# Optimization experiments

Hardware: AMD Instinct MI355X
Metric: run time of the kernel (lower is better)

Reference implementation:

```python
import jax, jax.numpy as jnp
import numpy as np

WIN_SIZE = 11
WIN_SIGMA = 1.5
DATA_RANGE = 1.0
K1, K2 = 0.01, 0.03


def _gauss_1d(size, sigma):
    coords = np.arange(size, dtype=np.float64) - size // 2
    g = np.exp(-(coords ** 2) / (2.0 * sigma ** 2))
    g = g / g.sum()
    return jnp.asarray(g, dtype=jnp.float32)


def _gaussian_filter(x, win1d):
    # x: (N, C, H, W); separable depthwise gaussian blur, VALID padding
    C = x.shape[1]
    dn = ('NCHW', 'OIHW', 'NCHW')
    kh = jnp.tile(win1d.reshape(1, 1, -1, 1), (C, 1, 1, 1))
    kw = jnp.tile(win1d.reshape(1, 1, 1, -1), (C, 1, 1, 1))
    x = jax.lax.conv_general_dilated(x, kh, (1, 1), 'VALID', dimension_numbers=dn, feature_group_count=C)
    x = jax.lax.conv_general_dilated(x, kw, (1, 1), 'VALID', dimension_numbers=dn, feature_group_count=C)
    return x


def setup_inputs() -> dict:
    key = jax.random.key(0)
    k1, k2 = jax.random.split(key)
    shape = (32, 1, 512, 512)
    y_pred = jax.random.uniform(k1, shape, dtype=jnp.float32)
    y_true = jax.random.uniform(k2, shape, dtype=jnp.float32)
    return {"y_pred": y_pred, "y_true": y_true}


def reference(y_pred, y_true):
    # SSIMLoss.forward: 1 - ssim(y_true, y_pred, data_range=1.0, size_average=True)
    C1 = (K1 * DATA_RANGE) ** 2
    C2 = (K2 * DATA_RANGE) ** 2
    win = _gauss_1d(WIN_SIZE, WIN_SIGMA)

    X, Y = y_true, y_pred
    mu1 = _gaussian_filter(X, win)
    mu2 = _gaussian_filter(Y, win)
    sigma1_sq = _gaussian_filter(X * X, win) - mu1 * mu1
    sigma2_sq = _gaussian_filter(Y * Y, win) - mu2 * mu2
    sigma12 = _gaussian_filter(X * Y, win) - mu1 * mu2

    cs_map = (2.0 * sigma12 + C2) / (sigma1_sq + sigma2_sq + C2)
    ssim_map = ((2.0 * mu1 * mu2 + C1) / (mu1 * mu1 + mu2 * mu2 + C1)) * cs_map
    # size_average=True -> mean over everything
    return 1.0 - jnp.mean(ssim_map)
```

## Files before the change

kernel.cpp:

```cpp
#include <hip/hip_runtime.h>
#include <cmath>

#define IMG      512
#define OUT      502
#define TW       64
#define TH       32
#define IW       74
#define PITCH    76
#define NTHREADS 256
#define TILES_X  8
#define TILES_Y  16
#define NIMG     32
#define NBLOCKS  (TILES_X * TILES_Y * NIMG)

struct GaussW { float w[11]; };

__global__ __launch_bounds__(NTHREADS, 4)
void ssim_tile_kernel(const float* __restrict__ ypred,
                      const float* __restrict__ ytrue,
                      float* __restrict__ partials,
                      GaussW gw)
{
    __shared__ __align__(16) float sV[5][TH * PITCH];
    __shared__ float wsum[4];

    const int t     = threadIdx.x;
    const int tileX = blockIdx.x, tileY = blockIdx.y, img = blockIdx.z;
    const int ox0   = tileX * TW;
    const int oy0   = tileY * TH;

    const float* __restrict__ Xp = ytrue + (size_t)img * IMG * IMG;
    const float* __restrict__ Yp = ypred + (size_t)img * IMG * IMG;

    if (t < IW * 3) {
        const int c    = t % IW;
        const int g    = t / IW;
        const int r0   = g * 11;
        const int jmax = (g == 2) ? 10 : 11;

        int gx = ox0 + c; if (gx > IMG - 1) gx = IMG - 1;
        const float* __restrict__ Xc = Xp + gx;
        const float* __restrict__ Yc = Yp + gx;

        float acc[5][11];
        #pragma unroll
        for (int m = 0; m < 5; ++m)
            #pragma unroll
            for (int j = 0; j < 11; ++j) acc[m][j] = 0.f;

        #pragma unroll
        for (int k = 0; k < 21; ++k) {
            int gy = oy0 + r0 + k; if (gy > IMG - 1) gy = IMG - 1;
            const float x = Xc[(size_t)gy * IMG];
            const float y = Yc[(size_t)gy * IMG];
            const float xx = x * x, yy = y * y, xy = x * y;
            #pragma unroll
            for (int j = 0; j < 11; ++j) {
                if (k - j >= 0 && k - j <= 10) {
                    const float w = gw.w[k - j];
                    acc[0][j] += w * x;
                    acc[1][j] += w * y;
                    acc[2][j] += w * xx;
                    acc[3][j] += w * yy;
                    acc[4][j] += w * xy;
                }
            }
        }

        #pragma unroll
        for (int j = 0; j < 11; ++j) {
            if (j < jmax) {
                const int o = (r0 + j) * PITCH + c;
                sV[0][o] = acc[0][j];
                sV[1][o] = acc[1][j];
                sV[2][o] = acc[2][j];
                sV[3][o] = acc[3][j];
                sV[4][o] = acc[4][j];
            }
        }
    }
    __syncthreads();

    const float C1 = 0.0001f;
    const float C2 = 0.0009f;
    float lsum = 0.f;

    #pragma unroll
    for (int it = 0; it < 2; ++it) {
        const int i   = t + it * NTHREADS;
        const int cg  = i & 15;
        const int row = i >> 4;

        float res[5][4];
        #pragma unroll
        for (int m = 0; m < 5; ++m) {
            const float4* p = reinterpret_cast<const float4*>(&sV[m][row * PITCH + cg * 4]);
            const float4 a = p[0], b = p[1], cq = p[2], d = p[3];
            const float win[16] = { a.x,  a.y,  a.z,  a.w,
                                    b.x,  b.y,  b.z,  b.w,
                                    cq.x, cq.y, cq.z, cq.w,
                                    d.x,  d.y,  d.z,  d.w };
            #pragma unroll
            for (int c = 0; c < 4; ++c) {
                float r = 0.f;
                #pragma unroll
                for (int k = 0; k < 11; ++k) r += gw.w[k] * win[c + k];
                res[m][c] = r;
            }
        }

        const int oy = oy0 + row;
        #pragma unroll
        for (int c = 0; c < 4; ++c) {
            const int ox = ox0 + cg * 4 + c;
            const float mu1 = res[0][c], mu2 = res[1][c];
            const float s1  = res[2][c] - mu1 * mu1;
            const float s2  = res[3][c] - mu2 * mu2;
            const float s12 = res[4][c] - mu1 * mu2;
            const float num = (2.f * mu1 * mu2 + C1) * (2.f * s12 + C2);
            const float den = (mu1 * mu1 + mu2 * mu2 + C1) * (s1 + s2 + C2);
            const float ssim = num / den;
            if (ox < OUT && oy < OUT) lsum += ssim;
        }
    }

    #pragma unroll
    for (int off = 32; off > 0; off >>= 1) lsum += __shfl_down(lsum, off, 64);
    if ((t & 63) == 0) wsum[t >> 6] = lsum;
    __syncthreads();
    if (t == 0) {
        const float b = wsum[0] + wsum[1] + wsum[2] + wsum[3];
        partials[((size_t)img * TILES_Y + tileY) * TILES_X + tileX] = b;
    }
}

__global__ void ssim_reduce_kernel(const float* __restrict__ partials,
                                   float* __restrict__ out)
{
    __shared__ double ws[4];
    const int t = threadIdx.x;
    double s = 0.0;
    for (int i = t; i < NBLOCKS; i += 256) s += (double)partials[i];
    #pragma unroll
    for (int off = 32; off > 0; off >>= 1) s += __shfl_down(s, off, 64);
    if ((t & 63) == 0) ws[t >> 6] = s;
    __syncthreads();
    if (t == 0) {
        const double total = ws[0] + ws[1] + ws[2] + ws[3];
        const double mean  = total / ((double)OUT * (double)OUT * (double)NIMG);
        out[0] = (float)(1.0 - mean);
    }
}

extern "C" void kernel_launch(void* const* d_in, const int* in_sizes, int n_in,
                              void* d_out, int out_size, void* d_ws, size_t ws_size,
                              hipStream_t stream)
{
    const float* ypred = (const float*)d_in[0];
    const float* ytrue = (const float*)d_in[1];
    float* out      = (float*)d_out;
    float* partials = (float*)d_ws;

    GaussW gw;
    double g[11], sum = 0.0;
    for (int i = 0; i < 11; ++i) {
        const double c = (double)i - 5.0;
        g[i] = std::exp(-(c * c) / (2.0 * 1.5 * 1.5));
        sum += g[i];
    }
    for (int i = 0; i < 11; ++i) gw.w[i] = (float)(g[i] / sum);

    dim3 grid(TILES_X, TILES_Y, NIMG);
    ssim_tile_kernel<<<grid, NTHREADS, 0, stream>>>(ypred, ytrue, partials, gw);
    ssim_reduce_kernel<<<1, 256, 0, stream>>>(partials, out);
}
```

Measured before the change: 130.1 us.

## Shift edge tiles inward and widen horizontal pass to 8 outputs per thread

Measured after the change: 127.4 us. 2.1% less time.

```diff
diff --git a/kernel.cpp b/kernel.cpp
--- a/kernel.cpp
+++ b/kernel.cpp
@@ -7,6 +7,7 @@
 #define TH       32
 #define IW       74
 #define PITCH    76
+#define MOFF     (TH * PITCH)
 #define NTHREADS 256
 #define TILES_X  8
 #define TILES_Y  16
@@ -15,32 +16,31 @@
 
 struct GaussW { float w[11]; };
 
-__global__ __launch_bounds__(NTHREADS, 4)
+__global__ __launch_bounds__(NTHREADS, 3)
 void ssim_tile_kernel(const float* __restrict__ ypred,
                       const float* __restrict__ ytrue,
                       float* __restrict__ partials,
                       GaussW gw)
 {
-    __shared__ __align__(16) float sV[5][TH * PITCH];
+    __shared__ __align__(16) float sV[5 * MOFF];
     __shared__ float wsum[4];
 
     const int t     = threadIdx.x;
     const int tileX = blockIdx.x, tileY = blockIdx.y, img = blockIdx.z;
-    const int ox0   = tileX * TW;
-    const int oy0   = tileY * TH;
+    const int ox0 = (tileX == TILES_X - 1) ? (OUT - TW) : tileX * TW;
+    const int oy0 = (tileY == TILES_Y - 1) ? (OUT - TH) : tileY * TH;
 
-    const float* __restrict__ Xp = ytrue + (size_t)img * IMG * IMG;
-    const float* __restrict__ Yp = ypred + (size_t)img * IMG * IMG;
+    const size_t imgoff = (size_t)img * (IMG * IMG);
+    const float* __restrict__ Xp = ytrue + imgoff;
+    const float* __restrict__ Yp = ypred + imgoff;
 
     if (t < IW * 3) {
-        const int c    = t % IW;
-        const int g    = t / IW;
-        const int r0   = g * 11;
-        const int jmax = (g == 2) ? 10 : 11;
+        const int c  = t % IW;
+        const int g  = t / IW;
+        const int r0 = g * 11;
 
-        int gx = ox0 + c; if (gx > IMG - 1) gx = IMG - 1;
-        const float* __restrict__ Xc = Xp + gx;
-        const float* __restrict__ Yc = Yp + gx;
+        const float* __restrict__ Xc = Xp + (size_t)(oy0 + r0) * IMG + (ox0 + c);
+        const float* __restrict__ Yc = Yp + (size_t)(oy0 + r0) * IMG + (ox0 + c);
 
         float acc[5][11];
         #pragma unroll
@@ -49,10 +49,9 @@
             for (int j = 0; j < 11; ++j) acc[m][j] = 0.f;
 
         #pragma unroll
-        for (int k = 0; k < 21; ++k) {
-            int gy = oy0 + r0 + k; if (gy > IMG - 1) gy = IMG - 1;
-            const float x = Xc[(size_t)gy * IMG];
-            const float y = Yc[(size_t)gy * IMG];
+        for (int k = 0; k < 20; ++k) {
+            const float x = Xc[k * IMG];
+            const float y = Yc[k * IMG];
             const float xx = x * x, yy = y * y, xy = x * y;
             #pragma unroll
             for (int j = 0; j < 11; ++j) {
@@ -66,62 +65,83 @@
                 }
             }
         }
+        if (g < 2) {
+            const float x = Xc[20 * IMG];
+            const float y = Yc[20 * IMG];
+            const float w = gw.w[10];
+            acc[0][10] += w * x;
+            acc[1][10] += w * y;
+            acc[2][10] += w * (x * x);
+            acc[3][10] += w * (y * y);
+            acc[4][10] += w * (x * y);
+        }
 
+        const int o0 = r0 * PITCH + c;
         #pragma unroll
-        for (int j = 0; j < 11; ++j) {
-            if (j < jmax) {
-                const int o = (r0 + j) * PITCH + c;
-                sV[0][o] = acc[0][j];
-                sV[1][o] = acc[1][j];
-                sV[2][o] = acc[2][j];
-                sV[3][o] = acc[3][j];
-                sV[4][o] = acc[4][j];
-            }
+        for (int j = 0; j < 10; ++j) {
+            const int o = o0 + j * PITCH;
+            sV[0 * MOFF + o] = acc[0][j];
+            sV[1 * MOFF + o] = acc[1][j];
+            sV[2 * MOFF + o] = acc[2][j];
+            sV[3 * MOFF + o] = acc[3][j];
+            sV[4 * MOFF + o] = acc[4][j];
+        }
+        if (g < 2) {
+            const int o = o0 + 10 * PITCH;
+            sV[0 * MOFF + o] = acc[0][10];
+            sV[1 * MOFF + o] = acc[1][10];
+            sV[2 * MOFF + o] = acc[2][10];
+            sV[3 * MOFF + o] = acc[3][10];
+            sV[4 * MOFF + o] = acc[4][10];
         }
     }
     __syncthreads();
 
     const float C1 = 0.0001f;
     const float C2 = 0.0009f;
+
+    const int row  = t & 31;
+    const int seg  = t >> 5;
+    const int base = row * PITCH + seg * 8;
+
+    float res[5][8];
+    #pragma unroll
+    for (int m = 0; m < 5; ++m) {
+        const float4 q0 = *reinterpret_cast<const float4*>(&sV[base + m * MOFF +  0]);
+        const float4 q1 = *reinterpret_cast<const float4*>(&sV[base + m * MOFF +  4]);
+        const float4 q2 = *reinterpret_cast<const float4*>(&sV[base + m * MOFF +  8]);
+        const float4 q3 = *reinterpret_cast<const float4*>(&sV[base + m * MOFF + 12]);
+        const float4 q4 = *reinterpret_cast<const float4*>(&sV[base + m * MOFF + 16]);
+        const float win[20] = { q0.x, q0.y, q0.z, q0.w,
+                                q1.x, q1.y, q1.z, q1.w,
+                                q2.x, q2.y, q2.z, q2.w,
+                                q3.x, q3.y, q3.z, q3.w,
+                                q4.x, q4.y, q4.z, q4.w };
+        #pragma unroll
+        for (int c = 0; c < 8; ++c) {
+            float r = 0.f;
+            #pragma unroll
+            for (int k = 0; k < 11; ++k) r += gw.w[k] * win[c + k];
+            res[m][c] = r;
+        }
+    }
+
+    const int  oy     = oy0 + row;
+    const bool rowown = (oy >= tileY * TH);
     float lsum = 0.f;
 
     #pragma unroll
-    for (int it = 0; it < 2; ++it) {
-        const int i   = t + it * NTHREADS;
-        const int cg  = i & 15;
-        const int row = i >> 4;
-
-        float res[5][4];
-        #pragma unroll
-        for (int m = 0; m < 5; ++m) {
-            const float4* p = reinterpret_cast<const float4*>(&sV[m][row * PITCH + cg * 4]);
-            const float4 a = p[0], b = p[1], cq = p[2], d = p[3];
-            const float win[16] = { a.x,  a.y,  a.z,  a.w,
-                                    b.x,  b.y,  b.z,  b.w,
-                                    cq.x, cq.y, cq.z, cq.w,
-                                    d.x,  d.y,  d.z,  d.w };
-            #pragma unroll
-            for (int c = 0; c < 4; ++c) {
-                float r = 0.f;
-                #pragma unroll
-                for (int k = 0; k < 11; ++k) r += gw.w[k] * win[c + k];
-                res[m][c] = r;
-            }
-        }
-
-        const int oy = oy0 + row;
-        #pragma unroll
-        for (int c = 0; c < 4; ++c) {
-            const int ox = ox0 + cg * 4 + c;
-            const float mu1 = res[0][c], mu2 = res[1][c];
-            const float s1  = res[2][c] - mu1 * mu1;
-            const float s2  = res[3][c] - mu2 * mu2;
-            const float s12 = res[4][c] - mu1 * mu2;
-            const float num = (2.f * mu1 * mu2 + C1) * (2.f * s12 + C2);
-            const float den = (mu1 * mu1 + mu2 * mu2 + C1) * (s1 + s2 + C2);
-            const float ssim = num / den;
-            if (ox < OUT && oy < OUT) lsum += ssim;
-        }
+    for (int c = 0; c < 8; ++c) {
+        const int  ox  = ox0 + seg * 8 + c;
+        const bool own = rowown && (ox >= tileX * TW);
+        const float mu1 = res[0][c], mu2 = res[1][c];
+        const float s1  = res[2][c] - mu1 * mu1;
+        const float s2  = res[3][c] - mu2 * mu2;
+        const float s12 = res[4][c] - mu1 * mu2;
+        const float num = (2.f * mu1 * mu2 + C1) * (2.f * s12 + C2);
+        const float den = (mu1 * mu1 + mu2 * mu2 + C1) * (s1 + s2 + C2);
+        const float ssim = num / den;
+        lsum += own ? ssim : 0.f;
     }
 
     #pragma unroll
```

## Compute separable Gaussian blur with bf16 MFMA using split hi/lo precision

Applied to the files above, without the earlier changes.

Measured after the change: 159.6 us. 22.7% more time.

```diff
diff --git a/kernel.cpp b/kernel.cpp
--- a/kernel.cpp
+++ b/kernel.cpp
@@ -2,135 +2,188 @@
 #include <cmath>
 
 #define IMG      512
-#define OUT      502
+#define OUTD     502
 #define TW       64
-#define TH       32
-#define IW       74
-#define PITCH    76
+#define TH       16
 #define NTHREADS 256
 #define TILES_X  8
-#define TILES_Y  16
+#define TILES_Y  32
 #define NIMG     32
 #define NBLOCKS  (TILES_X * TILES_Y * NIMG)
-
-struct GaussW { float w[11]; };
-
-__global__ __launch_bounds__(NTHREADS, 4)
-void ssim_tile_kernel(const float* __restrict__ ypred,
+#define HT_PITCH 32
+
+typedef float f32x4  __attribute__((ext_vector_type(4)));
+typedef short bf16x8 __attribute__((ext_vector_type(8)));
+
+struct WSplit { unsigned short hi[11]; unsigned short lo[11]; };
+
+union Frag { unsigned u[4]; bf16x8 v; };
+
+__device__ __forceinline__ unsigned fbits(float x) { return __builtin_bit_cast(unsigned, x); }
+__device__ __forceinline__ float truncbf(float x) {
+    return __builtin_bit_cast(float, fbits(x) & 0xFFFF0000u);
+}
+__device__ __forceinline__ unsigned pkhi(float a, float b) {
+    return (fbits(b) & 0xFFFF0000u) | (fbits(a) >> 16);
+}
+__device__ __forceinline__ void split8(const float* v, Frag& fh, Frag& fl) {
+    #pragma unroll
+    for (int j = 0; j < 4; ++j) {
+        const float a = v[2*j], b = v[2*j+1];
+        fh.u[j] = pkhi(a, b);
+        fl.u[j] = pkhi(a - truncbf(a), b - truncbf(b));
+    }
+}
+
+#define MFMA16 __builtin_amdgcn_mfma_f32_16x16x32_bf16
+
+__global__ __launch_bounds__(NTHREADS, 3)
+void ssim_mfma_kernel(const float* __restrict__ ypred,
                       const float* __restrict__ ytrue,
                       float* __restrict__ partials,
-                      GaussW gw)
+                      WSplit ws)
 {
-    __shared__ __align__(16) float sV[5][TH * PITCH];
+    __shared__ unsigned short Wh[16][32], Wl[16][32];
+    __shared__ unsigned short Hp[10][TW * HT_PITCH];
     __shared__ float wsum[4];
 
-    const int t     = threadIdx.x;
-    const int tileX = blockIdx.x, tileY = blockIdx.y, img = blockIdx.z;
-    const int ox0   = tileX * TW;
-    const int oy0   = tileY * TH;
-
-    const float* __restrict__ Xp = ytrue + (size_t)img * IMG * IMG;
-    const float* __restrict__ Yp = ypred + (size_t)img * IMG * IMG;
-
-    if (t < IW * 3) {
-        const int c    = t % IW;
-        const int g    = t / IW;
-        const int r0   = g * 11;
-        const int jmax = (g == 2) ? 10 : 11;
-
-        int gx = ox0 + c; if (gx > IMG - 1) gx = IMG - 1;
-        const float* __restrict__ Xc = Xp + gx;
-        const float* __restrict__ Yc = Yp + gx;
-
-        float acc[5][11];
-        #pragma unroll
-        for (int m = 0; m < 5; ++m)
-            #pragma unroll
-            for (int j = 0; j < 11; ++j) acc[m][j] = 0.f;
-
-        #pragma unroll
-        for (int k = 0; k < 21; ++k) {
-            int gy = oy0 + r0 + k; if (gy > IMG - 1) gy = IMG - 1;
-            const float x = Xc[(size_t)gy * IMG];
-            const float y = Yc[(size_t)gy * IMG];
-            const float xx = x * x, yy = y * y, xy = x * y;
-            #pragma unroll
-            for (int j = 0; j < 11; ++j) {
-                if (k - j >= 0 && k - j <= 10) {
-                    const float w = gw.w[k - j];
-                    acc[0][j] += w * x;
-                    acc[1][j] += w * y;
-                    acc[2][j] += w * xx;
-                    acc[3][j] += w * yy;
-                    acc[4][j] += w * xy;
-                }
-            }
+    const int t    = threadIdx.x;
+    const int w    = t >> 6;
+    const int lane = t & 63;
+    const int m16  = lane & 15;
+    const int g4   = lane >> 4;
+
+    const int ox0 = blockIdx.x * TW;
+    const int oy0 = blockIdx.y * TH;
+    const int img = blockIdx.z;
+
+    const size_t imgoff = (size_t)img * (IMG * IMG);
+    const float* __restrict__ Xp = ytrue + imgoff;
+    const float* __restrict__ Yp = ypred + imgoff;
+
+    #pragma unroll
+    for (int i = t; i < 512; i += NTHREADS) {
+        const int n = i >> 5, k = i & 31, j = k - n;
+        const bool in = (j >= 0) && (j <= 10);
+        Wh[n][k] = in ? ws.hi[j] : 0;
+        Wl[n][k] = in ? ws.lo[j] : 0;
+    }
+    __syncthreads();
+
+    Frag wfh, wfl;
+    wfh.v = *reinterpret_cast<const bf16x8*>(&Wh[m16][g4 * 8]);
+    wfl.v = *reinterpret_cast<const bf16x8*>(&Wl[m16][g4 * 8]);
+
+    #pragma unroll
+    for (int u = 0; u < 2; ++u) {
+        const int uid = w * 2 + u;
+        const int rg  = uid >> 2;
+        const int ncg = uid & 3;
+
+        const int lrow = rg * 16 + m16;
+        const int grow = min(oy0 + lrow, IMG - 1);
+        const float* __restrict__ Xr = Xp + (size_t)grow * IMG;
+        const float* __restrict__ Yr = Yp + (size_t)grow * IMG;
+        const int cb = ox0 + ncg * 16 + g4 * 8;
+
+        float xv[8], yv[8];
+        #pragma unroll
+        for (int j = 0; j < 4; ++j) {
+            const int c = min(cb + 2 * j, IMG - 2);
+            const float2 fx = *reinterpret_cast<const float2*>(Xr + c);
+            const float2 fy = *reinterpret_cast<const float2*>(Yr + c);
+            xv[2*j] = fx.x; xv[2*j+1] = fx.y;
+            yv[2*j] = fy.x; yv[2*j+1] = fy.y;
         }
 
-        #pragma unroll
-        for (int j = 0; j < 11; ++j) {
-            if (j < jmax) {
-                const int o = (r0 + j) * PITCH + c;
-                sV[0][o] = acc[0][j];
-                sV[1][o] = acc[1][j];
-                sV[2][o] = acc[2][j];
-                sV[3][o] = acc[3][j];
-                sV[4][o] = acc[4][j];
-            }
+        f32x4 acc[5];
+        #pragma unroll
+        for (int m = 0; m < 5; ++m) acc[m] = (f32x4){0.f, 0.f, 0.f, 0.f};
+
+        float pv[8];
+        Frag fh, fl;
+        split8(xv, fh, fl);
+        acc[0] = MFMA16(fh.v, wfh.v, acc[0], 0, 0, 0);
+        acc[0] = MFMA16(fl.v, wfh.v, acc[0], 0, 0, 0);
+        acc[0] = MFMA16(fh.v, wfl.v, acc[0], 0, 0, 0);
+        split8(yv, fh, fl);
+        acc[1] = MFMA16(fh.v, wfh.v, acc[1], 0, 0, 0);
+        acc[1] = MFMA16(fl.v, wfh.v, acc[1], 0, 0, 0);
+        acc[1] = MFMA16(fh.v, wfl.v, acc[1], 0, 0, 0);
+        #pragma unroll
+        for (int j = 0; j < 8; ++j) pv[j] = xv[j] * xv[j];
+        split8(pv, fh, fl);
+        acc[2] = MFMA16(fh.v, wfh.v, acc[2], 0, 0, 0);
+        acc[2] = MFMA16(fl.v, wfh.v, acc[2], 0, 0, 0);
+        acc[2] = MFMA16(fh.v, wfl.v, acc[2], 0, 0, 0);
+        #pragma unroll
+        for (int j = 0; j < 8; ++j) pv[j] = yv[j] * yv[j];
+        split8(pv, fh, fl);
+        acc[3] = MFMA16(fh.v, wfh.v, acc[3], 0, 0, 0);
+        acc[3] = MFMA16(fl.v, wfh.v, acc[3], 0, 0, 0);
+        acc[3] = MFMA16(fh.v, wfl.v, acc[3], 0, 0, 0);
+        #pragma unroll
+        for (int j = 0; j < 8; ++j) pv[j] = xv[j] * yv[j];
+        split8(pv, fh, fl);
+        acc[4] = MFMA16(fh.v, wfh.v, acc[4], 0, 0, 0);
+        acc[4] = MFMA16(fl.v, wfh.v, acc[4], 0, 0, 0);
+        acc[4] = MFMA16(fh.v, wfl.v, acc[4], 0, 0, 0);
+
+        const int col = ncg * 16 + m16;
+        const int r0  = rg * 16 + g4 * 4;
+        #pragma unroll
+        for (int m = 0; m < 5; ++m) {
+            const float d0 = acc[m][0], d1 = acc[m][1], d2 = acc[m][2], d3 = acc[m][3];
+            const unsigned h0 = pkhi(d0, d1), h1 = pkhi(d2, d3);
+            const unsigned l0 = pkhi(d0 - truncbf(d0), d1 - truncbf(d1));
+            const unsigned l1 = pkhi(d2 - truncbf(d2), d3 - truncbf(d3));
+            const unsigned off = col * HT_PITCH + (r0 ^ ((col & 3) << 3));
+            *reinterpret_cast<uint2*>(&Hp[m * 2    ][off]) = make_uint2(h0, h1);
+            *reinterpret_cast<uint2*>(&Hp[m * 2 + 1][off]) = make_uint2(l0, l1);
         }
     }
     __syncthreads();
 
-    const float C1 = 0.0001f;
-    const float C2 = 0.0009f;
+    const int cg0  = w * 16;
+    const int colL = cg0 + m16;
+    const unsigned roff = colL * HT_PITCH + ((g4 * 8) ^ ((colL & 3) << 3));
+
+    f32x4 acc2[5];
+    #pragma unroll
+    for (int m = 0; m < 5; ++m) {
+        Frag ah, al;
+        ah.v = *reinterpret_cast<const bf16x8*>(&Hp[m * 2    ][roff]);
+        al.v = *reinterpret_cast<const bf16x8*>(&Hp[m * 2 + 1][roff]);
+        f32x4 a = (f32x4){0.f, 0.f, 0.f, 0.f};
+        a = MFMA16(ah.v, wfh.v, a, 0, 0, 0);
+        a = MFMA16(al.v, wfh.v, a, 0, 0, 0);
+        a = MFMA16(ah.v, wfl.v, a, 0, 0, 0);
+        acc2[m] = a;
+    }
+
+    const float C1 = 0.0001f, C2 = 0.0009f;
+    const int orow = oy0 + m16;
     float lsum = 0.f;
-
-    #pragma unroll
-    for (int it = 0; it < 2; ++it) {
-        const int i   = t + it * NTHREADS;
-        const int cg  = i & 15;
-        const int row = i >> 4;
-
-        float res[5][4];
-        #pragma unroll
-        for (int m = 0; m < 5; ++m) {
-            const float4* p = reinterpret_cast<const float4*>(&sV[m][row * PITCH + cg * 4]);
-            const float4 a = p[0], b = p[1], cq = p[2], d = p[3];
-            const float win[16] = { a.x,  a.y,  a.z,  a.w,
-                                    b.x,  b.y,  b.z,  b.w,
-                                    cq.x, cq.y, cq.z, cq.w,
-                                    d.x,  d.y,  d.z,  d.w };
-            #pragma unroll
-            for (int c = 0; c < 4; ++c) {
-                float r = 0.f;
-                #pragma unroll
-                for (int k = 0; k < 11; ++k) r += gw.w[k] * win[c + k];
-                res[m][c] = r;
-            }
-        }
-
-        const int oy = oy0 + row;
-        #pragma unroll
-        for (int c = 0; c < 4; ++c) {
-            const int ox = ox0 + cg * 4 + c;
-            const float mu1 = res[0][c], mu2 = res[1][c];
-            const float s1  = res[2][c] - mu1 * mu1;
-            const float s2  = res[3][c] - mu2 * mu2;
-            const float s12 = res[4][c] - mu1 * mu2;
-            const float num = (2.f * mu1 * mu2 + C1) * (2.f * s12 + C2);
-            const float den = (mu1 * mu1 + mu2 * mu2 + C1) * (s1 + s2 + C2);
-            const float ssim = num / den;
-            if (ox < OUT && oy < OUT) lsum += ssim;
-        }
+    #pragma unroll
+    for (int i = 0; i < 4; ++i) {
+        const int ocol = ox0 + cg0 + g4 * 4 + i;
+        const float mu1 = acc2[0][i], mu2 = acc2[1][i];
+        const float s1  = acc2[2][i] - mu1 * mu1;
+        const float s2  = acc2[3][i] - mu2 * mu2;
+        const float s12 = acc2[4][i] - mu1 * mu2;
+        const float num = (2.f * mu1 * mu2 + C1) * (2.f * s12 + C2);
+        const float den = (mu1 * mu1 + mu2 * mu2 + C1) * (s1 + s2 + C2);
+        const float ssim = num * __builtin_amdgcn_rcpf(den);
+        lsum += (ocol < OUTD && orow < OUTD) ? ssim : 0.f;
     }
 
     #pragma unroll
     for (int off = 32; off > 0; off >>= 1) lsum += __shfl_down(lsum, off, 64);
-    if ((t & 63) == 0) wsum[t >> 6] = lsum;
+    if (lane == 0) wsum[w] = lsum;
     __syncthreads();
     if (t == 0) {
-        const float b = wsum[0] + wsum[1] + wsum[2] + wsum[3];
-        partials[((size_t)img * TILES_Y + tileY) * TILES_X + tileX] = b;
+        partials[((size_t)blockIdx.z * TILES_Y + blockIdx.y) * TILES_X + blockIdx.x]
+            = wsum[0] + wsum[1] + wsum[2] + wsum[3];
     }
 }
 
@@ -147,9 +200,16 @@
     __syncthreads();
     if (t == 0) {
         const double total = ws[0] + ws[1] + ws[2] + ws[3];
-        const double mean  = total / ((double)OUT * (double)OUT * (double)NIMG);
+        const double mean  = total / ((double)OUTD * (double)OUTD * (double)NIMG);
         out[0] = (float)(1.0 - mean);
     }
+}
+
+static inline unsigned short bf16_rne(float f) {
+    unsigned b;
+    __builtin_memcpy(&b, &f, 4);
+    const unsigned r = b + 0x7FFFu + ((b >> 16) & 1u);
+    return (unsigned short)(r >> 16);
 }
 
 extern "C" void kernel_launch(void* const* d_in, const int* in_sizes, int n_in,
@@ -161,16 +221,24 @@
     float* out      = (float*)d_out;
     float* partials = (float*)d_ws;
 
-    GaussW gw;
     double g[11], sum = 0.0;
     for (int i = 0; i < 11; ++i) {
         const double c = (double)i - 5.0;
         g[i] = std::exp(-(c * c) / (2.0 * 1.5 * 1.5));
         sum += g[i];
     }
-    for (int i = 0; i < 11; ++i) gw.w[i] = (float)(g[i] / sum);
+    WSplit wsp;
+    for (int i = 0; i < 11; ++i) {
+        const float wf = (float)(g[i] / sum);
+        const unsigned short hi = bf16_rne(wf);
+        const unsigned hb = ((unsigned)hi) << 16;
+        float hif;
+        __builtin_memcpy(&hif, &hb, 4);
+        wsp.hi[i] = hi;
+        wsp.lo[i] = bf16_rne(wf - hif);
+    }
 
     dim3 grid(TILES_X, TILES_Y, NIMG);
-    ssim_tile_kernel<<<grid, NTHREADS, 0, stream>>>(ypred, ytrue, partials, gw);
+    ssim_mfma_kernel<<<grid, NTHREADS, 0, stream>>>(ypred, ytrue, partials, wsp);
     ssim_reduce_kernel<<<1, 256, 0, stream>>>(partials, out);
 }
```

## Split tile into two half-passes with double-buffered shared memory and fused sums

Applied to the files above, without the earlier changes.

New measurement: 126.5 us. -2.8%, faster.

```diff
diff --git a/kernel.cpp b/kernel.cpp
--- a/kernel.cpp
+++ b/kernel.cpp
@@ -4,9 +4,10 @@
 #define IMG      512
 #define OUT      502
 #define TW       64
-#define TH       32
+#define THF      32
+#define HH       16
 #define IW       74
-#define PITCH    76
+#define P2       78
 #define NTHREADS 256
 #define TILES_X  8
 #define TILES_Y  16
@@ -21,117 +22,132 @@
                       float* __restrict__ partials,
                       GaussW gw)
 {
-    __shared__ __align__(16) float sV[5][TH * PITCH];
+    __shared__ __align__(16) float2 sXY[2][HH * P2];
+    __shared__ __align__(16) float2 sSP[2][HH * P2];
     __shared__ float wsum[4];
 
     const int t     = threadIdx.x;
-    const int tileX = blockIdx.x, tileY = blockIdx.y, img = blockIdx.z;
-    const int ox0   = tileX * TW;
-    const int oy0   = tileY * TH;
+    const int tileX = blockIdx.x, tileY = blockIdx.y;
+    const int ox0 = (tileX == TILES_X - 1) ? (OUT - TW)  : tileX * TW;
+    const int oy0 = (tileY == TILES_Y - 1) ? (OUT - THF) : tileY * THF;
 
-    const float* __restrict__ Xp = ytrue + (size_t)img * IMG * IMG;
-    const float* __restrict__ Yp = ypred + (size_t)img * IMG * IMG;
+    const size_t imgoff = (size_t)blockIdx.z * (IMG * IMG);
+    const float* __restrict__ Xp = ytrue + imgoff;
+    const float* __restrict__ Yp = ypred + imgoff;
 
-    if (t < IW * 3) {
-        const int c    = t % IW;
-        const int g    = t / IW;
-        const int r0   = g * 11;
-        const int jmax = (g == 2) ? 10 : 11;
+    const bool p1 = (t < 2 * IW);
+    const int  g  = (t >= IW) ? 1 : 0;
+    const int  c  = t - g * IW;
+    const int  r0 = g * 8;
+    const unsigned off0 = (unsigned)((oy0 + r0) * IMG + (ox0 + c));
+    const int  o0 = r0 * P2 + c;
 
-        int gx = ox0 + c; if (gx > IMG - 1) gx = IMG - 1;
-        const float* __restrict__ Xc = Xp + gx;
-        const float* __restrict__ Yc = Yp + gx;
-
-        float acc[5][11];
-        #pragma unroll
-        for (int m = 0; m < 5; ++m)
-            #pragma unroll
-            for (int j = 0; j < 11; ++j) acc[m][j] = 0.f;
-
-        #pragma unroll
-        for (int k = 0; k < 21; ++k) {
-            int gy = oy0 + r0 + k; if (gy > IMG - 1) gy = IMG - 1;
-            const float x = Xc[(size_t)gy * IMG];
-            const float y = Yc[(size_t)gy * IMG];
-            const float xx = x * x, yy = y * y, xy = x * y;
-            #pragma unroll
-            for (int j = 0; j < 11; ++j) {
-                if (k - j >= 0 && k - j <= 10) {
-                    const float w = gw.w[k - j];
-                    acc[0][j] += w * x;
-                    acc[1][j] += w * y;
-                    acc[2][j] += w * xx;
-                    acc[3][j] += w * yy;
-                    acc[4][j] += w * xy;
-                }
-            }
-        }
-
-        #pragma unroll
-        for (int j = 0; j < 11; ++j) {
-            if (j < jmax) {
-                const int o = (r0 + j) * PITCH + c;
-                sV[0][o] = acc[0][j];
-                sV[1][o] = acc[1][j];
-                sV[2][o] = acc[2][j];
-                sV[3][o] = acc[3][j];
-                sV[4][o] = acc[4][j];
-            }
-        }
-    }
-    __syncthreads();
+    const int prow = t & 15;
+    const int pseg = t >> 4;
+    const int pb   = prow * P2 + pseg * 4;
 
     const float C1 = 0.0001f;
     const float C2 = 0.0009f;
+
+    float xv[18], yv[18];
     float lsum = 0.f;
 
-    #pragma unroll
-    for (int it = 0; it < 2; ++it) {
-        const int i   = t + it * NTHREADS;
-        const int cg  = i & 15;
-        const int row = i >> 4;
+#define P1LOAD(OFF) do {                                                      \
+    _Pragma("unroll")                                                         \
+    for (int k = 0; k < 18; ++k) {                                            \
+        xv[k] = Xp[(OFF) + k * IMG];                                          \
+        yv[k] = Yp[(OFF) + k * IMG];                                          \
+    } } while (0)
 
-        float res[5][4];
-        #pragma unroll
-        for (int m = 0; m < 5; ++m) {
-            const float4* p = reinterpret_cast<const float4*>(&sV[m][row * PITCH + cg * 4]);
-            const float4 a = p[0], b = p[1], cq = p[2], d = p[3];
-            const float win[16] = { a.x,  a.y,  a.z,  a.w,
-                                    b.x,  b.y,  b.z,  b.w,
-                                    cq.x, cq.y, cq.z, cq.w,
-                                    d.x,  d.y,  d.z,  d.w };
-            #pragma unroll
-            for (int c = 0; c < 4; ++c) {
-                float r = 0.f;
-                #pragma unroll
-                for (int k = 0; k < 11; ++k) r += gw.w[k] * win[c + k];
-                res[m][c] = r;
-            }
-        }
+#define P1ACC(BUF) do {                                                       \
+    float aX[8], aY[8], aS[8], aP[8];                                         \
+    _Pragma("unroll")                                                         \
+    for (int j = 0; j < 8; ++j) { aX[j]=0.f; aY[j]=0.f; aS[j]=0.f; aP[j]=0.f; } \
+    _Pragma("unroll")                                                         \
+    for (int k = 0; k < 18; ++k) {                                            \
+        const float x = xv[k], y = yv[k];                                     \
+        const float s = __builtin_fmaf(y, y, x * x);             \
+        const float p = x * y;                                        \
+        _Pragma("unroll")                                                     \
+        for (int j = 0; j < 8; ++j) {                                         \
+            if (k - j >= 0 && k - j <= 10) {             \
+                const float w = gw.w[k - j];                                  \
+                aX[j] = __builtin_fmaf(w, x, aX[j]);                          \
+                aY[j] = __builtin_fmaf(w, y, aY[j]);                          \
+                aS[j] = __builtin_fmaf(w, s, aS[j]);                          \
+                aP[j] = __builtin_fmaf(w, p, aP[j]);                          \
+            }                                                                 \
+        }                                                                     \
+    }                                                                         \
+    _Pragma("unroll")                                                         \
+    for (int j = 0; j < 8; ++j) {                                             \
+        sXY[BUF][o0 + j * P2] = make_float2(aX[j], aY[j]);                    \
+        sSP[BUF][o0 + j * P2] = make_float2(aS[j], aP[j]);                    \
+    } } while (0)
 
-        const int oy = oy0 + row;
-        #pragma unroll
-        for (int c = 0; c < 4; ++c) {
-            const int ox = ox0 + cg * 4 + c;
-            const float mu1 = res[0][c], mu2 = res[1][c];
-            const float s1  = res[2][c] - mu1 * mu1;
-            const float s2  = res[3][c] - mu2 * mu2;
-            const float s12 = res[4][c] - mu1 * mu2;
-            const float num = (2.f * mu1 * mu2 + C1) * (2.f * s12 + C2);
-            const float den = (mu1 * mu1 + mu2 * mu2 + C1) * (s1 + s2 + C2);
-            const float ssim = num / den;
-            if (ox < OUT && oy < OUT) lsum += ssim;
-        }
-    }
+#define P2SSIM(BUF, H) do {                                                   \
+    float wA[14], wB[14];                                                     \
+    { const float4* q = reinterpret_cast<const float4*>(&sXY[BUF][pb]);       \
+      _Pragma("unroll")                                                       \
+      for (int i = 0; i < 7; ++i) { const float4 v = q[i];                    \
+          wA[2*i] = v.x; wB[2*i] = v.y; wA[2*i+1] = v.z; wB[2*i+1] = v.w; } } \
+    float mu1[4], mu2[4];                                                     \
+    _Pragma("unroll")                                                         \
+    for (int cc = 0; cc < 4; ++cc) {                                          \
+        float r1 = 0.f, r2 = 0.f;                                             \
+        _Pragma("unroll")                                                     \
+        for (int k = 0; k < 11; ++k) {                                        \
+            const float w = gw.w[k];                                          \
+            r1 = __builtin_fmaf(w, wA[cc + k], r1);                           \
+            r2 = __builtin_fmaf(w, wB[cc + k], r2);                           \
+        }                                                                     \
+        mu1[cc] = r1; mu2[cc] = r2;                                           \
+    }                                                                         \
+    { const float4* q = reinterpret_cast<const float4*>(&sSP[BUF][pb]);       \
+      _Pragma("unroll")                                                       \
+      for (int i = 0; i < 7; ++i) { const float4 v = q[i];                    \
+          wA[2*i] = v.x; wB[2*i] = v.y; wA[2*i+1] = v.z; wB[2*i+1] = v.w; } } \
+    const int  oyq    = oy0 + (H) * HH + prow;                                \
+    const bool rowown = (oyq >= tileY * THF);                                 \
+    _Pragma("unroll")                                                         \
+    for (int cc = 0; cc < 4; ++cc) {                                          \
+        float b3 = 0.f, b4 = 0.f;                                             \
+        _Pragma("unroll")                                                     \
+        for (int k = 0; k < 11; ++k) {                                        \
+            const float w = gw.w[k];                                          \
+            b3 = __builtin_fmaf(w, wA[cc + k], b3);          \
+            b4 = __builtin_fmaf(w, wB[cc + k], b4);          \
+        }                                                                     \
+        const int  oxq = ox0 + pseg * 4 + cc;                                 \
+        const bool own = rowown && (oxq >= tileX * TW);                       \
+        const float m1 = mu1[cc], m2 = mu2[cc];                               \
+        const float Pm = m1 * m2;                                             \
+        const float Sm = __builtin_fmaf(m1, m1, m2 * m2);                     \
+        const float num = __builtin_fmaf(2.f, Pm, C1)                         \
+                        * __builtin_fmaf(2.f, b4 - Pm, C2);                   \
+        const float den = (Sm + C1) * ((b3 + C2) - Sm);                       \
+        lsum += own ? num * __builtin_amdgcn_rcpf(den) : 0.f;                 \
+    } } while (0)
+
+    if (p1) { P1LOAD(off0); P1ACC(0); }
+    __syncthreads();
+    if (p1) { P1LOAD(off0 + HH * IMG); }
+    P2SSIM(0, 0);
+    if (p1) { P1ACC(1); }
+    __syncthreads();
+    P2SSIM(1, 1);
 
     #pragma unroll
     for (int off = 32; off > 0; off >>= 1) lsum += __shfl_down(lsum, off, 64);
     if ((t & 63) == 0) wsum[t >> 6] = lsum;
     __syncthreads();
     if (t == 0) {
-        const float b = wsum[0] + wsum[1] + wsum[2] + wsum[3];
-        partials[((size_t)img * TILES_Y + tileY) * TILES_X + tileX] = b;
+        partials[((size_t)blockIdx.z * TILES_Y + tileY) * TILES_X + tileX]
+            = wsum[0] + wsum[1] + wsum[2] + wsum[3];
     }
+#undef P1LOAD
+#undef P1ACC
+#undef P2SSIM
 }
 
 __global__ void ssim_reduce_kernel(const float* __restrict__ partials,
```
